# Optimization experiments

Hardware: AMD Instinct MI355X
Metric: run time of the kernel (lower is better)

The kernel has to match this reference:

```python
import jax, jax.numpy as jnp
import numpy as np

# ---- config (matches init_kwargs) ----
GROUP_NUM = 2048
K_NEIGHBORS = 32
OUT_DIM = 192
SIGMA, BASELINE, SCALING, EPS = 0.26, 0.1, 10.0, 1e-6
ALPHA, BETA = 1000.0, 100.0
ADAPTIVE_RATIO = 0.5
IN_DIM = 3
ADAPTIVE_DIM = int(OUT_DIM * ADAPTIVE_RATIO)          # 96
FOURIER_DIM = OUT_DIM - ADAPTIVE_DIM                  # 96
FEAT_DIM_F = FOURIER_DIM // (IN_DIM * 2)              # 16
FEAT_DIM_A = int(np.ceil(ADAPTIVE_DIM / IN_DIM))      # 32
FEAT_NUM_A = FEAT_DIM_A * IN_DIM                      # 96
OUT_IDX = np.linspace(0, FEAT_NUM_A - 1, ADAPTIVE_DIM).astype(np.int64)


def setup_inputs() -> dict:
    key = jax.random.key(0)
    k1, k2, k3, k4 = jax.random.split(key, 4)
    xyz = jax.random.normal(k1, (4, 8192, 3), dtype=jnp.float32)
    x = jax.random.normal(k2, (4, 8192, 96), dtype=jnp.float32)
    bn_gamma = jax.random.uniform(k3, (192,), dtype=jnp.float32)
    bn_beta = jax.random.normal(k4, (192,), dtype=jnp.float32)
    return {"xyz": xyz, "x": x, "bn_gamma": bn_gamma, "bn_beta": bn_beta}


def _fps(xyz, m):
    """Farthest point sampling. xyz: [B,N,3] -> idx [B,m] (int32). Seed = index 0."""
    def single(pts):
        n = pts.shape[0]
        def step(carry, _):
            dists, last = carry
            d = jnp.sum((pts - pts[last]) ** 2, axis=-1)
            dists = jnp.minimum(dists, d)
            nxt = jnp.argmax(dists).astype(jnp.int32)
            return (dists, nxt), nxt
        init = (jnp.full((n,), 1e10, pts.dtype), jnp.array(0, jnp.int32))
        _, idxs = jax.lax.scan(step, init, None, length=m - 1)
        return jnp.concatenate([jnp.zeros((1,), jnp.int32), idxs])
    return jax.vmap(single)(xyz)


def _square_distance(src, dst):
    # src: [B,S,3], dst: [B,N,3] -> [B,S,N]
    d = -2.0 * jnp.einsum('bsc,bnc->bsn', src, dst)
    d += jnp.sum(src ** 2, -1)[:, :, None]
    d += jnp.sum(dst ** 2, -1)[:, None, :]
    return d


def _gather_knn(points, idx):
    # points: [B,N,C], idx: [B,G,K] -> [B,G,K,C]
    return jax.vmap(lambda p, i: p[i])(points, idx)


def _forward(xyz, x, bn_gamma, bn_beta):
    B, N, _ = xyz.shape
    G, K = GROUP_NUM, K_NEIGHBORS

    # ---- Grouper_seg ----
    fps_idx = _fps(xyz, G)                                   # [B,G]
    lc_xyz = jnp.take_along_axis(xyz, fps_idx[..., None], 1)  # [B,G,3]
    lc_x = jnp.take_along_axis(x, fps_idx[..., None], 1)      # [B,G,C]
    sqr = _square_distance(lc_xyz, xyz)                       # [B,G,N]
    knn_idx = jax.lax.top_k(-sqr, K)[1]                       # [B,G,K] smallest-k
    knn_xyz = _gather_knn(xyz, knn_idx)                       # [B,G,K,3]
    knn_x = _gather_knn(x, knn_idx)                           # [B,G,K,C]

    # ---- Aggregation_seg: local normalization ----
    mean_x = lc_x[:, :, None, :]
    std_x = jnp.std(knn_x - mean_x, ddof=1)
    mean_xyz = lc_xyz[:, :, None, :]
    std_xyz = jnp.std(knn_xyz - mean_xyz, ddof=1)
    knn_x = (knn_x - mean_x) / (std_x + 1e-5)
    knn_xyz_n = (knn_xyz - mean_xyz) / (std_xyz + 1e-5)       # [B,G,K,3]
    C = knn_x.shape[-1]
    knn_x = jnp.concatenate(
        [knn_x, jnp.broadcast_to(lc_x[:, :, None, :], (B, G, K, C))], axis=-1)  # [B,G,K,2C]
    knn_xyz_cf = jnp.transpose(knn_xyz_n, (0, 3, 1, 2))       # [B,3,G,K]
    knn_x_cf = jnp.transpose(knn_x, (0, 3, 1, 2))             # [B,OUT_DIM,G,K]

    # ---- PosE_Geo: fourier part ----
    feat_range = jnp.arange(FEAT_DIM_F, dtype=knn_xyz_cf.dtype)
    dim_embed = ALPHA ** (feat_range / FEAT_DIM_F)            # [F]
    div = BETA * knn_xyz_cf[..., None] / dim_embed            # [B,3,G,K,F]
    fourier = jnp.stack([jnp.sin(div), jnp.cos(div)], axis=-1)  # [B,3,G,K,F,2]
    fourier = fourier.reshape(B, IN_DIM, G, K, 2 * FEAT_DIM_F)
    fourier = jnp.transpose(fourier, (0, 1, 4, 2, 3)).reshape(B, FOURIER_DIM, G, K)

    # ---- AdaptiveEmbedding (parameterless, data-driven) ----
    x4 = knn_xyz_n                                            # [B,G,K,3]
    gstd = jnp.mean(jnp.std(x4.reshape(B, -1, IN_DIM), axis=1, ddof=1))
    sig = SIGMA * (1.0 + gstd) + EPS
    blend = jax.nn.sigmoid((gstd - BASELINE) * SCALING)
    feat_val = jnp.linspace(-1.0, 1.0, FEAT_DIM_A + 2)[1:-1]  # [Fa]
    z = (x4[..., None] - feat_val) / sig                      # [B,G,K,3,Fa]
    comb = blend * jnp.exp(-0.5 * z * z) + (1.0 - blend) * jnp.cos(z)
    ae = comb.reshape(B, G, K, FEAT_NUM_A)[..., OUT_IDX]      # [B,G,K,ADAPTIVE_DIM]
    ae_cf = jnp.transpose(ae, (0, 3, 1, 2))                   # [B,ADAPTIVE_DIM,G,K]

    pe = jnp.concatenate([fourier, ae_cf], axis=1)            # [B,OUT_DIM,G,K]
    knn_x_w = (knn_x_cf + pe) * pe

    # ---- Pooling_seg: max+mean pool, BatchNorm1d (train stats) + GELU ----
    lc = jnp.max(knn_x_w, -1) + jnp.mean(knn_x_w, -1)         # [B,OUT_DIM,G]
    mu = jnp.mean(lc, axis=(0, 2), keepdims=True)
    var = jnp.var(lc, axis=(0, 2), keepdims=True)
    y = (lc - mu) / jnp.sqrt(var + 1e-5)
    y = y * bn_gamma[None, :, None] + bn_beta[None, :, None]
    return jax.nn.gelu(y, approximate=False)


def reference(xyz, x, bn_gamma, bn_beta):
    return _forward(xyz, x, bn_gamma, bn_beta)
```

## Files before the change

### kernel.cpp

```cpp
#include <hip/hip_runtime.h>
#include <cstdint>
#include <math.h>

#define NPTS 8192
#define NB 4
#define NG 2048
#define NK 32
#define CIN 96
#define COUT 192

typedef unsigned long long ull;

__global__ __launch_bounds__(256) void setup_kernel(const float* __restrict__ xyz,
                                                    float* __restrict__ xs, float* __restrict__ ys,
                                                    float* __restrict__ zs, float* __restrict__ d2){
  int i = blockIdx.x*256 + threadIdx.x;
  if (i >= NB*NPTS) return;
  float x = xyz[3*i+0], y = xyz[3*i+1], z = xyz[3*i+2];
  xs[i]=x; ys[i]=y; zs[i]=z;
  d2[i] = __fadd_rn(__fadd_rn(__fmul_rn(x,x),__fmul_rn(y,y)),__fmul_rn(z,z));
}

template<int CTRL>
__device__ __forceinline__ float dppmaxf(float v){
  int o = __builtin_amdgcn_update_dpp(__float_as_int(v), __float_as_int(v), CTRL, 0xf, 0xf, false);
  return fmaxf(v, __int_as_float(o));
}
template<int CTRL>
__device__ __forceinline__ unsigned dppmaxu(unsigned v){
  unsigned o = (unsigned)__builtin_amdgcn_update_dpp((int)v, (int)v, CTRL, 0xf, 0xf, false);
  return (o > v) ? o : v;
}
__device__ __forceinline__ float wavemaxf(float v){
  v = dppmaxf<0x111>(v); v = dppmaxf<0x112>(v); v = dppmaxf<0x114>(v);
  v = dppmaxf<0x118>(v); v = dppmaxf<0x142>(v); v = dppmaxf<0x143>(v);
  return v;
}
__device__ __forceinline__ unsigned wavemaxu(unsigned v){
  v = dppmaxu<0x111>(v); v = dppmaxu<0x112>(v); v = dppmaxu<0x114>(v);
  v = dppmaxu<0x118>(v); v = dppmaxu<0x142>(v); v = dppmaxu<0x143>(v);
  return v;
}

__global__ __launch_bounds__(512,2) void fps_kernel(const float* __restrict__ xyz, int* __restrict__ fps_idx){
#pragma clang fp contract(off)
  extern __shared__ char smem[];
  float4* ctab = (float4*)smem;
  ull*    keys = (ull*)(smem + 131072);
  int*    hist = (int*)(smem + 131072 + 128);
  float*  bbs  = (float*)(smem + 131072 + 128 + 2048);
  const int b = blockIdx.x, t = threadIdx.x;
  const int w = t>>6, lane = t&63;
  const float* base = xyz + (size_t)b*NPTS*3;

  float ox[16], oy[16], oz[16];
#pragma unroll
  for (int j=0;j<16;++j){
    int p = t + 512*j;
    ox[j]=base[3*p+0]; oy[j]=base[3*p+1]; oz[j]=base[3*p+2];
  }
  float mnx=ox[0],mxx=ox[0],mny=oy[0],mxy=oy[0],mnz=oz[0],mxz=oz[0];
#pragma unroll
  for (int j=1;j<16;++j){
    mnx=fminf(mnx,ox[j]); mxx=fmaxf(mxx,ox[j]);
    mny=fminf(mny,oy[j]); mxy=fmaxf(mxy,oy[j]);
    mnz=fminf(mnz,oz[j]); mxz=fmaxf(mxz,oz[j]);
  }
#pragma unroll
  for (int off=32; off>0; off>>=1){
    mnx=fminf(mnx,__shfl_xor(mnx,off)); mxx=fmaxf(mxx,__shfl_xor(mxx,off));
    mny=fminf(mny,__shfl_xor(mny,off)); mxy=fmaxf(mxy,__shfl_xor(mxy,off));
    mnz=fminf(mnz,__shfl_xor(mnz,off)); mxz=fmaxf(mxz,__shfl_xor(mxz,off));
  }
  hist[t] = 0;
  if (lane==0){
    bbs[w*6+0]=mnx; bbs[w*6+1]=mxx; bbs[w*6+2]=mny;
    bbs[w*6+3]=mxy; bbs[w*6+4]=mnz; bbs[w*6+5]=mxz;
  }
  if (t==0) fps_idx[b*NG] = 0;
  __syncthreads();
  float gx0=1e30f,gx1=-1e30f,gy0=1e30f,gy1=-1e30f,gz0=1e30f,gz1=-1e30f;
  for (int q=0;q<8;++q){
    gx0=fminf(gx0,bbs[q*6+0]); gx1=fmaxf(gx1,bbs[q*6+1]);
    gy0=fminf(gy0,bbs[q*6+2]); gy1=fmaxf(gy1,bbs[q*6+3]);
    gz0=fminf(gz0,bbs[q*6+4]); gz1=fmaxf(gz1,bbs[q*6+5]);
  }
  const float sxv = 8.0f/fmaxf(gx1-gx0,1e-20f);
  const float syv = 8.0f/fmaxf(gy1-gy0,1e-20f);
  const float szv = 8.0f/fmaxf(gz1-gz0,1e-20f);
  int cell[16];
#pragma unroll
  for (int j=0;j<16;++j){
    int cx = min(7,(int)((ox[j]-gx0)*sxv));
    int cy = min(7,(int)((oy[j]-gy0)*syv));
    int cz = min(7,(int)((oz[j]-gz0)*szv));
    int m = (cx&1) | ((cy&1)<<1) | ((cz&1)<<2)
          | ((cx&2)<<2) | ((cy&2)<<3) | ((cz&2)<<4)
          | ((cx&4)<<4) | ((cy&4)<<5) | ((cz&4)<<6);
    cell[j]=m;
    atomicAdd(&hist[m],1);
  }
  __syncthreads();
  if (t==0){
    int run=0;
    for (int c=0;c<512;++c){ int h=hist[c]; hist[c]=run; run+=h; }
  }
  __syncthreads();
#pragma unroll
  for (int j=0;j<16;++j){
    int pos = atomicAdd(&hist[cell[j]],1);
    ctab[pos] = make_float4(ox[j],oy[j],oz[j], __int_as_float(t+512*j));
  }
  __syncthreads();
  float px[16],py[16],pz[16],D[16]; unsigned lowb[16];
  float bx0,bx1,by0,by1,bz0,bz1;
#pragma unroll
  for (int j=0;j<16;++j){
    int pos = (w<<10) + (j<<6) + lane;
    float4 c4 = ctab[pos];
    px[j]=c4.x; py[j]=c4.y; pz[j]=c4.z;
    unsigned orig = (unsigned)__float_as_int(c4.w);
    lowb[j] = ((8191u-orig)<<13) | (unsigned)pos;
    D[j] = 1e10f;
    if (j==0){ bx0=c4.x; bx1=c4.x; by0=c4.y; by1=c4.y; bz0=c4.z; bz1=c4.z; }
    else {
      bx0=fminf(bx0,c4.x); bx1=fmaxf(bx1,c4.x);
      by0=fminf(by0,c4.y); by1=fmaxf(by1,c4.y);
      bz0=fminf(bz0,c4.z); bz1=fmaxf(bz1,c4.z);
    }
  }
#pragma unroll
  for (int off=32; off>0; off>>=1){
    bx0=fminf(bx0,__shfl_xor(bx0,off)); bx1=fmaxf(bx1,__shfl_xor(bx1,off));
    by0=fminf(by0,__shfl_xor(by0,off)); by1=fmaxf(by1,__shfl_xor(by1,off));
    bz0=fminf(bz0,__shfl_xor(bz0,off)); bz1=fmaxf(bz1,__shfl_xor(bz1,off));
  }

  float lx=base[0], ly=base[1], lz=base[2];
  float Mw = 1e10f;
  unsigned mylow = 0;
  for (int it=0; it<NG-1; ++it){
    float qx=fminf(fmaxf(lx,bx0),bx1);
    float qy=fminf(fmaxf(ly,by0),by1);
    float qz=fminf(fmaxf(lz,bz0),bz1);
    float ddx=qx-lx, ddy=qy-ly, ddz=qz-lz;
    float LB = (ddx*ddx+ddy*ddy)+ddz*ddz;
    ull* kslot = &keys[(it&1)*8 + w];
    if (LB <= Mw*1.0001f){
      float bd=-1.0f;
#pragma unroll
      for (int j=0;j<16;++j){
        float dx=px[j]-lx, dy=py[j]-ly, dz=pz[j]-lz;
        float d=(dx*dx+dy*dy)+dz*dz;
        float nd=fminf(D[j],d);
        D[j]=nd;
        bd=fmaxf(bd,nd);
      }
      unsigned bl=0;
#pragma unroll
      for (int j=0;j<16;++j){
        unsigned c2 = (lowb[j]>bl)?lowb[j]:bl;
        bl = (D[j]==bd) ? c2 : bl;
      }
      float m = wavemaxf(bd);
      float bdw = __int_as_float(__builtin_amdgcn_readlane(__float_as_int(m),63));
      unsigned cand = (bd==bdw) ? bl : 0u;
      unsigned mu = wavemaxu(cand);
      if (lane==63) *kslot = (((ull)__float_as_uint(bdw))<<32) | (ull)mu;
      Mw = bdw;
      mylow = (unsigned)__builtin_amdgcn_readlane((int)mu,63);
    } else {
      if (lane==63) *kslot = (((ull)__float_as_uint(Mw))<<32) | (ull)mylow;
    }
    __syncthreads();
    const ull* kk = keys + (it&1)*8;
    ull k = kk[0];
#pragma unroll
    for (int q=1;q<8;++q){ ull o=kk[q]; if (o>k) k=o; }
    unsigned lw = (unsigned)k;
    float4 c4 = ctab[lw & 0x1FFFu];
    lx=c4.x; ly=c4.y; lz=c4.z;
    if (t==0) fps_idx[b*NG + it + 1] = (int)(8191u - ((lw>>13)&0x1FFFu));
  }
}

__device__ __forceinline__ bool lexlt(float ad, int ai, float bd, int bi){
  return (ad < bd) || ((ad == bd) && (ai < bi));
}
__device__ __forceinline__ void sort_desc(float& d, int& i, int lane){
#pragma unroll
  for (int k=2;k<=64;k<<=1){
#pragma unroll
    for (int j=k>>1;j>0;j>>=1){
      float od = __shfl_xor(d, j);
      int   oi = __shfl_xor(i, j);
      bool dirUp = (lane & k) != 0;
      bool lower = (lane & j) == 0;
      bool less  = lexlt(d,i,od,oi);
      bool keep  = (less == (lower == dirUp));
      if (!keep){ d=od; i=oi; }
    }
  }
}
__device__ __forceinline__ void merge_asc(float& d, int& i, int lane){
#pragma unroll
  for (int j=32;j>0;j>>=1){
    float od = __shfl_xor(d, j);
    int   oi = __shfl_xor(i, j);
    bool lower = (lane & j) == 0;
    bool less  = lexlt(d,i,od,oi);
    bool keep  = (less == lower);
    if (!keep){ d=od; i=oi; }
  }
}

__global__ __launch_bounds__(256) void knn_kernel(const float* __restrict__ xs, const float* __restrict__ ys,
                                                  const float* __restrict__ zs, const float* __restrict__ d2,
                                                  const int* __restrict__ fps_idx, int* __restrict__ knn_out){
  __shared__ float tx[256], ty[256], tz[256], td[256];
  const int tid = threadIdx.x;
  const int wid = tid>>6, lane = tid&63;
  const int pid = blockIdx.x*4 + wid;
  const int b = pid >> 11;
  const float* bx = xs + b*NPTS;
  const float* by = ys + b*NPTS;
  const float* bz = zs + b*NPTS;
  const float* bD = d2 + b*NPTS;
  const int fi = fps_idx[pid];
  const float ax = bx[fi], ay = by[fi], az = bz[fi];
  const float src2 = __fadd_rn(__fadd_rn(__fmul_rn(ax,ax),__fmul_rn(ay,ay)),__fmul_rn(az,az));
  float Ad = INFINITY; int Ai = 0x7fffffff;
  float tau_d = INFINITY; int tau_i = 0x7fffffff;
  for (int s=0; s<NPTS/256; ++s){
    __syncthreads();
    int gidx = s*256 + tid;
    tx[tid]=bx[gidx]; ty[tid]=by[gidx]; tz[tid]=bz[gidx]; td[tid]=bD[gidx];
    __syncthreads();
    float m0,m1,m2,m3; int i0,i1,i2,i3;
#define LOADJ(mj, ij, J) { int li = (J)*64 + lane; \
    float dot = __fadd_rn(__fadd_rn(__fmul_rn(ax,tx[li]),__fmul_rn(ay,ty[li])),__fmul_rn(az,tz[li])); \
    mj = __fadd_rn(__fadd_rn(__fmul_rn(-2.0f,dot), src2), td[li]); ij = s*256 + li; }
    LOADJ(m0,i0,0) LOADJ(m1,i1,1) LOADJ(m2,i2,2) LOADJ(m3,i3,3)
#undef LOADJ
    while (true){
      bool any = lexlt(m0,i0,tau_d,tau_i) || lexlt(m1,i1,tau_d,tau_i) ||
                 lexlt(m2,i2,tau_d,tau_i) || lexlt(m3,i3,tau_d,tau_i);
      if (__ballot(any) == 0ull) break;
      float cd = m0; int ci = i0; int sel = 0;
      if (lexlt(m1,i1,cd,ci)){ cd=m1; ci=i1; sel=1; }
      if (lexlt(m2,i2,cd,ci)){ cd=m2; ci=i2; sel=2; }
      if (lexlt(m3,i3,cd,ci)){ cd=m3; ci=i3; sel=3; }
      if      (sel==0) m0=INFINITY;
      else if (sel==1) m1=INFINITY;
      else if (sel==2) m2=INFINITY;
      else             m3=INFINITY;
      sort_desc(cd, ci, lane);
      if (lexlt(cd,ci,Ad,Ai)){ Ad=cd; Ai=ci; }
      merge_asc(Ad, Ai, lane);
      tau_d = __shfl(Ad, 31);
      tau_i = __shfl(Ai, 31);
    }
  }
  if (lane < NK) knn_out[pid*NK + lane] = Ai;
}

__global__ __launch_bounds__(256) void stats_kernel(const float* __restrict__ x, const float* __restrict__ xyz,
                                                    const int* __restrict__ fps_idx, const int* __restrict__ knn,
                                                    double* __restrict__ partials){
  const int tid=threadIdx.x, wid=tid>>6, lane=tid&63;
  const int pid = blockIdx.x*4 + wid;
  const int b = pid>>11;
  const int fi = fps_idx[pid];
  const float* xb = x + (size_t)b*NPTS*CIN;
  const float* zb = xyz + (size_t)b*NPTS*3;
  const float lc0 = xb[fi*CIN + lane];
  float lc1 = 0.f; if (lane<32) lc1 = xb[fi*CIN + 64 + lane];
  float czv = 0.f; if (lane<3)  czv = zb[fi*3 + lane];
  double s1=0.0, s2=0.0, a1=0.0, a2=0.0;
  for (int k=0;k<NK;++k){
    int idx = knn[pid*NK + k];
    float d0 = __fsub_rn(xb[idx*CIN + lane], lc0);
    s1 += (double)d0; s2 += (double)d0*(double)d0;
    if (lane<32){
      float d1 = __fsub_rn(xb[idx*CIN + 64 + lane], lc1);
      s1 += (double)d1; s2 += (double)d1*(double)d1;
    }
    if (lane<3){
      float w = __fsub_rn(zb[idx*3 + lane], czv);
      a1 += (double)w; a2 += (double)w*(double)w;
    }
  }
#pragma unroll
  for (int off=32; off>0; off>>=1){ s1 += __shfl_xor(s1,off); s2 += __shfl_xor(s2,off); }
  __shared__ double shx[4][2];
  __shared__ double shz[4][3][2];
  if (lane==0){ shx[wid][0]=s1; shx[wid][1]=s2; }
  if (lane<3){ shz[wid][lane][0]=a1; shz[wid][lane][1]=a2; }
  __syncthreads();
  if (tid==0){
    double u0=0,u1=0;
    for (int w=0;w<4;++w){ u0+=shx[w][0]; u1+=shx[w][1]; }
    double* outp = partials + (size_t)blockIdx.x*8;
    outp[0]=u0; outp[1]=u1;
    for (int axq=0; axq<3; ++axq){
      double v0=0,v1=0;
      for (int w=0;w<4;++w){ v0+=shz[w][axq][0]; v1+=shz[w][axq][1]; }
      outp[2+2*axq]=v0; outp[3+2*axq]=v1;
    }
  }
}

__global__ void finalize_kernel(const double* __restrict__ partials, float* __restrict__ scal){
  const int lane = threadIdx.x;
  double s1=0,s2=0;
  double z0a=0,z0b=0,z1a=0,z1b=0,z2a=0,z2b=0;
  for (int i=0;i<32;++i){
    const double* p = partials + (size_t)(lane*32+i)*8;
    s1+=p[0]; s2+=p[1];
    z0a+=p[2]; z0b+=p[3]; z1a+=p[4]; z1b+=p[5]; z2a+=p[6]; z2b+=p[7];
  }
#pragma unroll
  for (int off=32; off>0; off>>=1){ s1+=__shfl_xor(s1,off); s2+=__shfl_xor(s2,off); }
#pragma unroll
  for (int off=8; off>0; off>>=1){
    z0a+=__shfl_xor(z0a,off); z0b+=__shfl_xor(z0b,off);
    z1a+=__shfl_xor(z1a,off); z1b+=__shfl_xor(z1b,off);
    z2a+=__shfl_xor(z2a,off); z2b+=__shfl_xor(z2b,off);
  }
  __shared__ double zb[4][3][2];
  if ((lane&15)==0){
    int b = lane>>4;
    zb[b][0][0]=z0a; zb[b][0][1]=z0b;
    zb[b][1][0]=z1a; zb[b][1][1]=z1b;
    zb[b][2][0]=z2a; zb[b][2][1]=z2b;
  }
  __syncthreads();
  if (lane==0){
    double nx = (double)NB*NG*NK*CIN;
    double varx = (s2 - s1*s1/nx)/(nx-1.0);
    float stdx = (float)sqrt(varx);
    double t1=0,t2=0;
    for (int b=0;b<4;++b) for (int a=0;a<3;++a){ t1+=zb[b][a][0]; t2+=zb[b][a][1]; }
    double nz = (double)NB*NG*NK*3;
    double varz = (t2 - t1*t1/nz)/(nz-1.0);
    float stdz = (float)sqrt(varz);
    float sdiv = stdz + 1e-5f;
    double n2 = (double)NG*NK;
    double acc=0.0;
    for (int b=0;b<4;++b) for (int a=0;a<3;++a){
      double v = (zb[b][a][1] - zb[b][a][0]*zb[b][a][0]/n2)/(n2-1.0);
      acc += sqrt(v);
    }
    float gstd = (float)(acc/12.0) / sdiv;
    float sig = 0.26f*(1.0f+gstd) + 1e-6f;
    float blend = 1.0f/(1.0f + expf(-(gstd-0.1f)*10.0f));
    scal[0] = 1.0f/(stdx + 1e-5f);
    scal[1] = 1.0f/sdiv;
    scal[2] = 1.0f/sig;
    scal[3] = blend;
  }
}

__global__ __launch_bounds__(256) void main_kernel(const float* __restrict__ x, const float* __restrict__ xyz,
                                                   const int* __restrict__ fps_idx, const int* __restrict__ knn,
                                                   const float* __restrict__ scal, float* __restrict__ lc_out){
  const int tid=threadIdx.x, wid=tid>>6, lane=tid&63;
  const int pid = blockIdx.x*4 + wid;
  const int b = pid>>11, g = pid&2047;
  const float inv_x = scal[0], inv_z = scal[1], inv_sig = scal[2], blend = scal[3];
  const float omb = 1.0f - blend;
  const int fi = fps_idx[pid];
  const float* xb = x + (size_t)b*NPTS*CIN;
  const float* zb = xyz + (size_t)b*NPTS*3;
  const float cx = zb[fi*3+0], cy = zb[fi*3+1], cz = zb[fi*3+2];
  const float lcx0 = xb[fi*CIN + lane];
  const float lcx1 = (lane<32) ? xb[fi*CIN + 64 + lane] : xb[fi*CIN + lane - 32];
  const float lcx2 = xb[fi*CIN + 32 + lane];
  const int dim0 = lane>>5;
  const int rr0 = lane&31;
  const bool cos0 = rr0 & 1;
  const float bs0 = 100.0f / powf(1000.0f, (float)(rr0>>1) * (1.0f/16.0f));
  const bool cos1 = lane & 1;
  const float bs1 = 100.0f / powf(1000.0f, (float)((lane&31)>>1) * (1.0f/16.0f));
  const float fv1 = (float)(-1.0 + 2.0*(double)(lane-32+1)/33.0);
  const int dim2 = (32+lane)>>5;
  const int j2 = (32+lane)&31;
  const float fv2 = (float)(-1.0 + 2.0*(double)(j2+1)/33.0);

  float mx0=-INFINITY, mx1=-INFINITY, mx2=-INFINITY;
  float sm0=0.f, sm1=0.f, sm2=0.f;
  for (int k=0;k<NK;++k){
    const int idx = knn[pid*NK + k];
    const float p0 = zb[idx*3+0], p1 = zb[idx*3+1], p2v = zb[idx*3+2];
    const float xn0 = (p0-cx)*inv_z, xn1 = (p1-cy)*inv_z, xn2 = (p2v-cz)*inv_z;
    const float xk0 = xb[idx*CIN + lane];
    float xk1 = 0.f; if (lane<32) xk1 = xb[idx*CIN + 64 + lane];
    {
      float v = dim0 ? xn1 : xn0;
      float a = v * bs0;
      float pe = cos0 ? __cosf(a) : __sinf(a);
      float f = (xk0 - lcx0) * inv_x;
      float w = (f + pe) * pe;
      mx0 = fmaxf(mx0, w); sm0 += w;
    }
    {
      float pe, f;
      if (lane < 32){
        float a = xn2 * bs1;
        pe = cos1 ? __cosf(a) : __sinf(a);
        f = (xk1 - lcx1) * inv_x;
      } else {
        float zq = (xn0 - fv1) * inv_sig;
        pe = blend * __expf(-0.5f*zq*zq) + omb * __cosf(zq);
        f = lcx1;
      }
      float w = (f + pe) * pe;
      mx1 = fmaxf(mx1, w); sm1 += w;
    }
    {
      float v = (dim2==1) ? xn1 : xn2;
      float zq = (v - fv2) * inv_sig;
      float pe = blend * __expf(-0.5f*zq*zq) + omb * __cosf(zq);
      float w = (lcx2 + pe) * pe;
      mx2 = fmaxf(mx2, w); sm2 += w;
    }
  }
  const size_t obase = ((size_t)b*COUT)*NG + g;
  lc_out[obase + (size_t)lane*NG]       = mx0 + sm0*(1.0f/32.0f);
  lc_out[obase + (size_t)(64+lane)*NG]  = mx1 + sm1*(1.0f/32.0f);
  lc_out[obase + (size_t)(128+lane)*NG] = mx2 + sm2*(1.0f/32.0f);
}

__global__ __launch_bounds__(256) void bn_stats_kernel(const float* __restrict__ lc, float* __restrict__ bn){
  const int c = blockIdx.x, t = threadIdx.x, lane=t&63, wid=t>>6;
  double s1=0.0, s2=0.0;
  for (int i=t; i<NB*NG; i+=256){
    int b=i>>11, g=i&2047;
    float v = lc[((size_t)(b*COUT)+c)*NG + g];
    s1 += (double)v; s2 += (double)v*(double)v;
  }
#pragma unroll
  for (int off=32; off>0; off>>=1){ s1+=__shfl_xor(s1,off); s2+=__shfl_xor(s2,off); }
  __shared__ double sh1[4], sh2[4];
  if (lane==0){ sh1[wid]=s1; sh2[wid]=s2; }
  __syncthreads();
  if (t==0){
    double a=sh1[0]+sh1[1]+sh1[2]+sh1[3], q=sh2[0]+sh2[1]+sh2[2]+sh2[3];
    double n=(double)(NB*NG);
    double mu=a/n, var=q/n - mu*mu;
    bn[c]=(float)mu;
    bn[COUT+c]=(float)(1.0/sqrt(var + 1e-5));
  }
}

__global__ __launch_bounds__(256) void final_kernel(const float* __restrict__ bn, const float* __restrict__ gamma,
                                                    const float* __restrict__ beta, float* __restrict__ out){
  int i = blockIdx.x*256 + threadIdx.x;
  int c = (i >> 11) % COUT;
  float v = out[i];
  float y = (v - bn[c]) * bn[COUT + c];
  y = y*gamma[c] + beta[c];
  out[i] = y * 0.5f * (1.0f + erff(y * 0.70710678118654752f));
}

extern "C" void kernel_launch(void* const* d_in, const int* in_sizes, int n_in,
                              void* d_out, int out_size, void* d_ws, size_t ws_size,
                              hipStream_t stream){
  const float* xyz   = (const float*)d_in[0];
  const float* x     = (const float*)d_in[1];
  const float* gamma = (const float*)d_in[2];
  const float* beta  = (const float*)d_in[3];
  float* out = (float*)d_out;
  char* ws = (char*)d_ws;
  int*    fps  = (int*)   (ws + 0);
  int*    knn  = (int*)   (ws + 32768);
  float*  xs   = (float*) (ws + 1081344);
  float*  ys   = (float*) (ws + 1212416);
  float*  zs   = (float*) (ws + 1343488);
  float*  d2   = (float*) (ws + 1474560);
  double* parts= (double*)(ws + 1605632);
  float*  scal = (float*) (ws + 1736704);
  float*  bn   = (float*) (ws + 1736768);

  const int fps_lds = 131072 + 128 + 2048 + 192;
  (void)hipFuncSetAttribute(reinterpret_cast<const void*>(fps_kernel),
                            hipFuncAttributeMaxDynamicSharedMemorySize, fps_lds);

  setup_kernel   <<<dim3((NB*NPTS+255)/256), dim3(256), 0, stream>>>(xyz, xs, ys, zs, d2);
  fps_kernel     <<<dim3(NB),                dim3(512), fps_lds, stream>>>(xyz, fps);
  knn_kernel     <<<dim3(NB*NG/4),           dim3(256), 0, stream>>>(xs, ys, zs, d2, fps, knn);
  stats_kernel   <<<dim3(NB*NG/4),           dim3(256), 0, stream>>>(x, xyz, fps, knn, parts);
  finalize_kernel<<<dim3(1),                 dim3(64),  0, stream>>>(parts, scal);
  main_kernel    <<<dim3(NB*NG/4),           dim3(256), 0, stream>>>(x, xyz, fps, knn, scal, out);
  bn_stats_kernel<<<dim3(COUT),              dim3(256), 0, stream>>>(out, bn);
  final_kernel   <<<dim3((NB*COUT*NG)/256),  dim3(256), 0, stream>>>(bn, gamma, beta, out);
}
```

Before: 2.433 ms.

## Double FPS block to 1024 threads, fuse key/index wave reduction, parallel prefix scan

The farthest-point-sampling kernel now runs 16 waves of 1024 threads, each holding 8 points instead of 16, so the serial per-iteration distance update is shorter per wave. The two separate wave-max reductions (distance, then index) are merged into one DPP pass over a (distance, index) pair. The serial single-thread histogram scan is replaced by a 64-lane shuffle scan. In exchange, each iteration's cross-wave key merge reads 16 slots instead of 8, and the barrier now synchronises twice as many waves.

```diff
diff --git a/kernel.cpp b/kernel.cpp
--- a/kernel.cpp
+++ b/kernel.cpp
@@ -22,46 +22,34 @@
 }
 
 template<int CTRL>
-__device__ __forceinline__ float dppmaxf(float v){
-  int o = __builtin_amdgcn_update_dpp(__float_as_int(v), __float_as_int(v), CTRL, 0xf, 0xf, false);
-  return fmaxf(v, __int_as_float(o));
-}
-template<int CTRL>
-__device__ __forceinline__ unsigned dppmaxu(unsigned v){
-  unsigned o = (unsigned)__builtin_amdgcn_update_dpp((int)v, (int)v, CTRL, 0xf, 0xf, false);
-  return (o > v) ? o : v;
-}
-__device__ __forceinline__ float wavemaxf(float v){
-  v = dppmaxf<0x111>(v); v = dppmaxf<0x112>(v); v = dppmaxf<0x114>(v);
-  v = dppmaxf<0x118>(v); v = dppmaxf<0x142>(v); v = dppmaxf<0x143>(v);
-  return v;
-}
-__device__ __forceinline__ unsigned wavemaxu(unsigned v){
-  v = dppmaxu<0x111>(v); v = dppmaxu<0x112>(v); v = dppmaxu<0x114>(v);
-  v = dppmaxu<0x118>(v); v = dppmaxu<0x142>(v); v = dppmaxu<0x143>(v);
-  return v;
-}
-
-__global__ __launch_bounds__(512,2) void fps_kernel(const float* __restrict__ xyz, int* __restrict__ fps_idx){
+__device__ __forceinline__ void dppmax_pair(unsigned& hi, unsigned& lo){
+  unsigned ohi = (unsigned)__builtin_amdgcn_update_dpp((int)hi, (int)hi, CTRL, 0xf, 0xf, false);
+  unsigned olo = (unsigned)__builtin_amdgcn_update_dpp((int)lo, (int)lo, CTRL, 0xf, 0xf, false);
+  bool gt = (ohi > hi) || (ohi == hi && olo > lo);
+  hi = gt ? ohi : hi;
+  lo = gt ? olo : lo;
+}
+
+__global__ __launch_bounds__(1024,4) void fps_kernel(const float* __restrict__ xyz, int* __restrict__ fps_idx){
 #pragma clang fp contract(off)
   extern __shared__ char smem[];
   float4* ctab = (float4*)smem;
   ull*    keys = (ull*)(smem + 131072);
-  int*    hist = (int*)(smem + 131072 + 128);
-  float*  bbs  = (float*)(smem + 131072 + 128 + 2048);
+  int*    hist = (int*)(smem + 131072 + 256);
+  float*  bbs  = (float*)(smem + 131072 + 256 + 2048);
   const int b = blockIdx.x, t = threadIdx.x;
   const int w = t>>6, lane = t&63;
   const float* base = xyz + (size_t)b*NPTS*3;
 
-  float ox[16], oy[16], oz[16];
-#pragma unroll
-  for (int j=0;j<16;++j){
-    int p = t + 512*j;
+  float ox[8], oy[8], oz[8];
+#pragma unroll
+  for (int j=0;j<8;++j){
+    int p = t + 1024*j;
     ox[j]=base[3*p+0]; oy[j]=base[3*p+1]; oz[j]=base[3*p+2];
   }
   float mnx=ox[0],mxx=ox[0],mny=oy[0],mxy=oy[0],mnz=oz[0],mxz=oz[0];
 #pragma unroll
-  for (int j=1;j<16;++j){
+  for (int j=1;j<8;++j){
     mnx=fminf(mnx,ox[j]); mxx=fmaxf(mxx,ox[j]);
     mny=fminf(mny,oy[j]); mxy=fmaxf(mxy,oy[j]);
     mnz=fminf(mnz,oz[j]); mxz=fmaxf(mxz,oz[j]);
@@ -72,7 +60,7 @@
     mny=fminf(mny,__shfl_xor(mny,off)); mxy=fmaxf(mxy,__shfl_xor(mxy,off));
     mnz=fminf(mnz,__shfl_xor(mnz,off)); mxz=fmaxf(mxz,__shfl_xor(mxz,off));
   }
-  hist[t] = 0;
+  if (t < 512) hist[t] = 0;
   if (lane==0){
     bbs[w*6+0]=mnx; bbs[w*6+1]=mxx; bbs[w*6+2]=mny;
     bbs[w*6+3]=mxy; bbs[w*6+4]=mnz; bbs[w*6+5]=mxz;
@@ -80,7 +68,7 @@
   if (t==0) fps_idx[b*NG] = 0;
   __syncthreads();
   float gx0=1e30f,gx1=-1e30f,gy0=1e30f,gy1=-1e30f,gz0=1e30f,gz1=-1e30f;
-  for (int q=0;q<8;++q){
+  for (int q=0;q<16;++q){
     gx0=fminf(gx0,bbs[q*6+0]); gx1=fmaxf(gx1,bbs[q*6+1]);
     gy0=fminf(gy0,bbs[q*6+2]); gy1=fmaxf(gy1,bbs[q*6+3]);
     gz0=fminf(gz0,bbs[q*6+4]); gz1=fmaxf(gz1,bbs[q*6+5]);
@@ -88,9 +76,9 @@
   const float sxv = 8.0f/fmaxf(gx1-gx0,1e-20f);
   const float syv = 8.0f/fmaxf(gy1-gy0,1e-20f);
   const float szv = 8.0f/fmaxf(gz1-gz0,1e-20f);
-  int cell[16];
-#pragma unroll
-  for (int j=0;j<16;++j){
+  int cell[8];
+#pragma unroll
+  for (int j=0;j<8;++j){
     int cx = min(7,(int)((ox[j]-gx0)*sxv));
     int cy = min(7,(int)((oy[j]-gy0)*syv));
     int cz = min(7,(int)((oz[j]-gz0)*szv));
@@ -101,32 +89,46 @@
     atomicAdd(&hist[m],1);
   }
   __syncthreads();
-  if (t==0){
-    int run=0;
-    for (int c=0;c<512;++c){ int h=hist[c]; hist[c]=run; run+=h; }
-  }
-  __syncthreads();
-#pragma unroll
-  for (int j=0;j<16;++j){
+  if (t < 64){
+    int s0[8];
+#pragma unroll
+    for (int j=0;j<8;++j) s0[j]=hist[t*8+j];
+    int tot=0;
+#pragma unroll
+    for (int j=0;j<8;++j){ int v=s0[j]; s0[j]=tot; tot+=v; }
+    int inc=tot;
+#pragma unroll
+    for (int off=1; off<64; off<<=1){
+      int o=__shfl_up(inc,off);
+      if (t>=off) inc+=o;
+    }
+    int excl=inc-tot;
+#pragma unroll
+    for (int j=0;j<8;++j) hist[t*8+j]=excl+s0[j];
+  }
+  __syncthreads();
+#pragma unroll
+  for (int j=0;j<8;++j){
     int pos = atomicAdd(&hist[cell[j]],1);
-    ctab[pos] = make_float4(ox[j],oy[j],oz[j], __int_as_float(t+512*j));
-  }
-  __syncthreads();
-  float px[16],py[16],pz[16],D[16]; unsigned lowb[16];
+    ctab[pos] = make_float4(ox[j],oy[j],oz[j], __int_as_float(t+1024*j));
+  }
+  __syncthreads();
+  float px[8],py[8],pz[8],D[8]; unsigned lowb[8];
   float bx0,bx1,by0,by1,bz0,bz1;
 #pragma unroll
-  for (int j=0;j<16;++j){
-    int pos = (w<<10) + (j<<6) + lane;
+  for (int j=0;j<8;++j){
+    int pos = (w<<9) + (j<<6) + lane;
     float4 c4 = ctab[pos];
     px[j]=c4.x; py[j]=c4.y; pz[j]=c4.z;
     unsigned orig = (unsigned)__float_as_int(c4.w);
     lowb[j] = ((8191u-orig)<<13) | (unsigned)pos;
     D[j] = 1e10f;
-    if (j==0){ bx0=c4.x; bx1=c4.x; by0=c4.y; by1=c4.y; bz0=c4.z; bz1=c4.z; }
+    asm volatile("" : "+v"(px[j]), "+v"(py[j]), "+v"(pz[j]), "+v"(lowb[j]));
+    if (j==0){ bx0=px[j]; bx1=px[j]; by0=py[j]; by1=py[j]; bz0=pz[j]; bz1=pz[j]; }
     else {
-      bx0=fminf(bx0,c4.x); bx1=fmaxf(bx1,c4.x);
-      by0=fminf(by0,c4.y); by1=fmaxf(by1,c4.y);
-      bz0=fminf(bz0,c4.z); bz1=fmaxf(bz1,c4.z);
+      bx0=fminf(bx0,px[j]); bx1=fmaxf(bx1,px[j]);
+      by0=fminf(by0,py[j]); by1=fmaxf(by1,py[j]);
+      bz0=fminf(bz0,pz[j]); bz1=fmaxf(bz1,pz[j]);
     }
   }
 #pragma unroll
@@ -145,11 +147,11 @@
     float qz=fminf(fmaxf(lz,bz0),bz1);
     float ddx=qx-lx, ddy=qy-ly, ddz=qz-lz;
     float LB = (ddx*ddx+ddy*ddy)+ddz*ddz;
-    ull* kslot = &keys[(it&1)*8 + w];
+    ull* kslot = &keys[(it&1)*16 + w];
     if (LB <= Mw*1.0001f){
       float bd=-1.0f;
 #pragma unroll
-      for (int j=0;j<16;++j){
+      for (int j=0;j<8;++j){
         float dx=px[j]-lx, dy=py[j]-ly, dz=pz[j]-lz;
         float d=(dx*dx+dy*dy)+dz*dz;
         float nd=fminf(D[j],d);
@@ -158,25 +160,26 @@
       }
       unsigned bl=0;
 #pragma unroll
-      for (int j=0;j<16;++j){
+      for (int j=0;j<8;++j){
         unsigned c2 = (lowb[j]>bl)?lowb[j]:bl;
         bl = (D[j]==bd) ? c2 : bl;
       }
-      float m = wavemaxf(bd);
-      float bdw = __int_as_float(__builtin_amdgcn_readlane(__float_as_int(m),63));
-      unsigned cand = (bd==bdw) ? bl : 0u;
-      unsigned mu = wavemaxu(cand);
-      if (lane==63) *kslot = (((ull)__float_as_uint(bdw))<<32) | (ull)mu;
-      Mw = bdw;
-      mylow = (unsigned)__builtin_amdgcn_readlane((int)mu,63);
+      unsigned hi = __float_as_uint(bd), lo = bl;
+      dppmax_pair<0x111>(hi,lo); dppmax_pair<0x112>(hi,lo); dppmax_pair<0x114>(hi,lo);
+      dppmax_pair<0x118>(hi,lo); dppmax_pair<0x142>(hi,lo); dppmax_pair<0x143>(hi,lo);
+      unsigned hw  = (unsigned)__builtin_amdgcn_readlane((int)hi,63);
+      unsigned lwv = (unsigned)__builtin_amdgcn_readlane((int)lo,63);
+      if (lane==63) *kslot = (((ull)hw)<<32) | (ull)lwv;
+      Mw = __uint_as_float(hw);
+      mylow = lwv;
     } else {
       if (lane==63) *kslot = (((ull)__float_as_uint(Mw))<<32) | (ull)mylow;
     }
     __syncthreads();
-    const ull* kk = keys + (it&1)*8;
+    const ull* kk = keys + (it&1)*16;
     ull k = kk[0];
 #pragma unroll
-    for (int q=1;q<8;++q){ ull o=kk[q]; if (o>k) k=o; }
+    for (int q=1;q<16;++q){ ull o=kk[q]; if (o>k) k=o; }
     unsigned lw = (unsigned)k;
     float4 c4 = ctab[lw & 0x1FFFu];
     lx=c4.x; ly=c4.y; lz=c4.z;
@@ -482,12 +485,12 @@
   float*  scal = (float*) (ws + 1736704);
   float*  bn   = (float*) (ws + 1736768);
 
-  const int fps_lds = 131072 + 128 + 2048 + 192;
+  const int fps_lds = 131072 + 256 + 2048 + 384;
   (void)hipFuncSetAttribute(reinterpret_cast<const void*>(fps_kernel),
                             hipFuncAttributeMaxDynamicSharedMemorySize, fps_lds);
 
   setup_kernel   <<<dim3((NB*NPTS+255)/256), dim3(256), 0, stream>>>(xyz, xs, ys, zs, d2);
-  fps_kernel     <<<dim3(NB),                dim3(512), fps_lds, stream>>>(xyz, fps);
+  fps_kernel     <<<dim3(NB),                dim3(1024), fps_lds, stream>>>(xyz, fps);
   knn_kernel     <<<dim3(NB*NG/4),           dim3(256), 0, stream>>>(xs, ys, zs, d2, fps, knn);
   stats_kernel   <<<dim3(NB*NG/4),           dim3(256), 0, stream>>>(x, xyz, fps, knn, parts);
   finalize_kernel<<<dim3(1),                 dim3(64),  0, stream>>>(parts, scal);
```

Measured after the change: 3.001 ms. +23.4%, slower.
